# Kernel optimization log

Hardware: AMD Instinct MI355X
Metric: run time of the kernel (lower is better)

## Reference

```python
import jax, jax.numpy as jnp
import numpy as np

DIM = 1024
HEADS = 16


def setup_inputs() -> dict:
    key = jax.random.key(0)
    ks = jax.random.split(key, 9)
    B, N, C = 2, 2048, DIM
    hd = C // HEADS
    s = 1.0 / np.sqrt(C)
    x = jax.random.normal(ks[0], (B, N, C), dtype=jnp.float32)
    wq = jax.random.normal(ks[1], (C, C), dtype=jnp.float32) * s
    wk = jax.random.normal(ks[2], (C, C), dtype=jnp.float32) * s
    wv = jax.random.normal(ks[3], (C, C), dtype=jnp.float32) * s
    wp = jax.random.normal(ks[4], (C, C), dtype=jnp.float32) * s
    bp = jnp.zeros((C,), dtype=jnp.float32)
    # rotary table: angles theta_j = 10000^{-2j/hd}, positions 0..N-1
    inv_freq = 1.0 / (10000.0 ** (jnp.arange(0, hd, 2, dtype=jnp.float32) / hd))
    ang = jnp.arange(N, dtype=jnp.float32)[:, None] * inv_freq[None, :]  # (N, hd//2)
    cos = jnp.cos(ang)
    sin = jnp.sin(ang)
    return {"x": x, "wq": wq, "wk": wk, "wv": wv, "wp": wp, "bp": bp,
            "cos": cos, "sin": sin, "num_heads": HEADS}


def _apply_rotary(t, cos, sin):
    # t: (B, N, H, D); cos/sin: (N, D//2) -> broadcast (1, N, 1, D//2)
    B, N, H, D = t.shape
    tr = t.reshape(B, N, H, D // 2, 2)
    t1, t2 = tr[..., 0], tr[..., 1]
    c = cos[None, :, None, :]
    s = sin[None, :, None, :]
    o1 = t1 * c - t2 * s
    o2 = t1 * s + t2 * c
    return jnp.stack([o1, o2], axis=-1).reshape(B, N, H, D)


def reference(x, wq, wk, wv, wp, bp, cos, sin, num_heads):
    B, N, C = x.shape
    H = num_heads
    D = C // H
    q = (x @ wq.T).reshape(B, N, H, D)
    k = (x @ wk.T).reshape(B, N, H, D)
    v = (x @ wv.T).reshape(B, N, H, D)
    q = _apply_rotary(q, cos, sin)
    k = _apply_rotary(k, cos, sin)
    scale = 1.0 / jnp.sqrt(jnp.asarray(D, dtype=x.dtype))
    # scores: (B, H, N, N)
    scores = jnp.einsum('bnhd,bmhd->bhnm', q, k) * scale
    attn = jax.nn.softmax(scores, axis=-1)
    out = jnp.einsum('bhnm,bmhd->bnhd', attn, v).reshape(B, N, C)
    return out @ wp.T + bp
```

## Files before the change

### kernel.cpp

```cpp
#include <hip/hip_runtime.h>
#include <hip/hip_bf16.h>
#include <stdint.h>

#define DEVI __device__ __forceinline__

using bf16 = __hip_bfloat16;
typedef __bf16 bf16x8 __attribute__((ext_vector_type(8)));
typedef float f32x4 __attribute__((ext_vector_type(4)));
typedef float f32x16 __attribute__((ext_vector_type(16)));
typedef int i32x2 __attribute__((ext_vector_type(2)));

static constexpr int Bb = 2, Nn = 2048, Cc = 1024, Hh = 16, Dd = 64;
static constexpr float CSC = 0.125f * 1.44269504088896340736f;

DEVI bf16 f2bf(float x) { __bf16 h = (__bf16)x; return *(bf16*)&h; }
DEVI float fexp2(float x) { return __builtin_amdgcn_exp2f(x); }

DEVI bf16x8 cvt8(f32x4 a, f32x4 b) {
  bf16x8 r;
  r[0] = (__bf16)a[0]; r[1] = (__bf16)a[1]; r[2] = (__bf16)a[2]; r[3] = (__bf16)a[3];
  r[4] = (__bf16)b[0]; r[5] = (__bf16)b[1]; r[6] = (__bf16)b[2]; r[7] = (__bf16)b[3];
  return r;
}

DEVI uint32_t pk2(float a, float b) {
  __bf16 x = (__bf16)a, y = (__bf16)b;
  uint16_t ux = *(uint16_t*)&x, uy = *(uint16_t*)&y;
  return (uint32_t)ux | ((uint32_t)uy << 16);
}

DEVI bf16x8 mk8(uint32_t a, uint32_t b, uint32_t c, uint32_t d) {
  union { uint32_t u[4]; bf16x8 v; } x;
  x.u[0] = a; x.u[1] = b; x.u[2] = c; x.u[3] = d;
  return x.v;
}

DEVI void gld_lds16(const bf16* g, bf16* l) {
  __builtin_amdgcn_global_load_lds(
      (__attribute__((address_space(1))) void*)(g),
      (__attribute__((address_space(3))) void*)(l),
      16, 0, 0);
}

__global__ __launch_bounds__(256) void k_cvt(const float* __restrict__ x,
                                             const float* __restrict__ wq,
                                             const float* __restrict__ wk,
                                             const float* __restrict__ wv,
                                             const float* __restrict__ wp,
                                             bf16* xb, bf16* wqb, bf16* wkb,
                                             bf16* wvb, bf16* wpb) {
  int bid = blockIdx.x;
  const float* src; bf16* dst; size_t off;
  if (bid < 2048) {
    src = x; dst = xb; off = (size_t)bid * 2048;
  } else {
    int s = (bid - 2048) >> 9, r = (bid - 2048) & 511;
    off = (size_t)r * 2048;
    src = s == 0 ? wq : s == 1 ? wk : s == 2 ? wv : wp;
    dst = s == 0 ? wqb : s == 1 ? wkb : s == 2 ? wvb : wpb;
  }
  size_t i = off + (size_t)threadIdx.x * 8;
  f32x4 a = *(const f32x4*)(src + i);
  f32x4 b = *(const f32x4*)(src + i + 4);
  *(bf16x8*)(dst + i) = cvt8(a, b);
}

template <int MFC, class Epi>
DEVI void gemm_lds_body(const bf16* __restrict__ A, const bf16* __restrict__ Bw,
                        int K, int m0, int n0, bf16* lA, bf16* lB, Epi epi) {
  constexpr int BM = MFC * 32;
  constexpr int PA = BM / 64;
  const int t = threadIdx.x;
  const int lane = t & 63, wave = t >> 6;
  const int wr = wave >> 1, wc = wave & 1;

  f32x4 acc[MFC][4] = {};

  for (int k0 = 0; k0 < K; k0 += 32) {
    __syncthreads();
#pragma unroll
    for (int p = 0; p < PA; ++p) {
      int c = p * 256 + t;
      int row = c >> 2, col = (c & 3) * 8;
      gld_lds16(A + (size_t)(m0 + row) * K + k0 + col,
                lA + (size_t)(p * 256 + wave * 64) * 8);
    }
#pragma unroll
    for (int p = 0; p < 2; ++p) {
      int c = p * 256 + t;
      int row = c >> 2, col = (c & 3) * 8;
      gld_lds16(Bw + (size_t)(n0 + row) * K + k0 + col,
                lB + (size_t)(p * 256 + wave * 64) * 8);
    }
    __syncthreads();

    bf16x8 aF[MFC];
#pragma unroll
    for (int mf = 0; mf < MFC; ++mf)
      aF[mf] = *(const bf16x8*)(lA + (wr * (BM / 2) + mf * 16 + (lane & 15)) * 32 + (lane >> 4) * 8);
#pragma unroll
    for (int nf = 0; nf < 4; ++nf) {
      bf16x8 bF = *(const bf16x8*)(lB + (wc * 64 + nf * 16 + (lane & 15)) * 32 + (lane >> 4) * 8);
#pragma unroll
      for (int mf = 0; mf < MFC; ++mf)
        acc[mf][nf] = __builtin_amdgcn_mfma_f32_16x16x32_bf16(aF[mf], bF, acc[mf][nf], 0, 0, 0);
    }
  }

#pragma unroll
  for (int mf = 0; mf < MFC; ++mf)
#pragma unroll
    for (int nf = 0; nf < 4; ++nf)
#pragma unroll
      for (int r = 0; r < 4; ++r) {
        int gm = m0 + wr * (BM / 2) + mf * 16 + (lane >> 4) * 4 + r;
        int gn = n0 + wc * 64 + nf * 16 + (lane & 15);
        epi(gm, gn, acc[mf][nf][r]);
      }
}

struct EpiRope {
  bf16* dst; const float* cosw; const float* sinw; float scale;
  DEVI void operator()(int gm, int gn, float v) const {
    int b = gm >> 11, n = gm & 2047;
    int h = gn >> 6, d = gn & 63;
    int i = d >> 1;
    float c = cosw[n * 32 + i], s = sinw[n * 32 + i];
    float p = __shfl_xor(v, 1);
    float o = (d & 1) ? (p * s + v * c) : (v * c - p * s);
    dst[((size_t)(b * Hh + h) * Nn + n) * 64 + d] = f2bf(o * scale);
  }
};

struct EpiVt {
  bf16* dst;
  DEVI void operator()(int gm, int gn, float v) const {
    int h = gm >> 6, d = gm & 63;
    int b = gn >> 11, n = gn & 2047;
    dst[((size_t)(b * Hh + h) * 64 + d) * Nn + n] = f2bf(v);
  }
};

struct EpiProj {
  float* dst; const float* bias;
  DEVI void operator()(int gm, int gn, float v) const {
    dst[(size_t)gm * Cc + gn] = v + bias[gn];
  }
};

__global__ __launch_bounds__(256) void k_qkv(const bf16* __restrict__ xb,
                                             const bf16* __restrict__ wqb,
                                             const bf16* __restrict__ wkb,
                                             const bf16* __restrict__ wvb,
                                             bf16* q_ws, bf16* k_ws, bf16* vt_ws,
                                             const float* __restrict__ cw,
                                             const float* __restrict__ sw) {
  __shared__ __align__(16) bf16 smem[256 * 32];
  bf16* lA = smem;
  bf16* lB = smem + 128 * 32;
  int bid = blockIdx.x;
  if (bid < 512) {
    int sub = bid & 255;
    int c = sub & 7, rest = sub >> 3;
    int m0 = (c + 8 * (rest & 3)) * 128;
    int n0 = (rest >> 2) * 128;
    bool isq = bid < 256;
    gemm_lds_body<4>(xb, isq ? wqb : wkb, Cc, m0, n0, lA, lB,
                     EpiRope{isq ? q_ws : k_ws, cw, sw, isq ? CSC : 1.0f});
  } else {
    int sub = bid - 512;
    int c = sub & 7, rest = sub >> 3;
    int n0 = (c + 8 * (rest & 3)) * 128;
    int m0 = (rest >> 2) * 128;
    gemm_lds_body<4>(wvb, xb, Cc, m0, n0, lA, lB, EpiVt{vt_ws});
  }
}

__global__ __launch_bounds__(256) void k_proj(const bf16* __restrict__ A,
                                              const bf16* __restrict__ W,
                                              float* dst, const float* __restrict__ bias) {
  __shared__ __align__(16) bf16 smem[192 * 32];
  gemm_lds_body<2>(A, W, Cc, blockIdx.x * 64, blockIdx.y * 128,
                   smem, smem + 64 * 32, EpiProj{dst, bias});
}

__global__ __launch_bounds__(512) void k_flash(const bf16* __restrict__ q_ws,
                                               const bf16* __restrict__ k_ws,
                                               const bf16* __restrict__ vt_ws,
                                               bf16* __restrict__ attn_o) {
  __shared__ __align__(16) bf16 lK[2][64 * 64];
  __shared__ __align__(16) bf16 lV[2][64 * 64];

  const int t = threadIdx.x, lane = t & 63, wave = t >> 6;
  const int l31 = lane & 31, hi = lane >> 5;
  const int bid = blockIdx.x;
  const int slot = bid >> 3;
  const int bh = (bid & 7) * 4 + (slot >> 3);
  const int q0w = (slot & 7) * 256 + wave * 32;
  const bf16* qg = q_ws + (size_t)bh * Nn * 64;
  const bf16* kg = k_ws + (size_t)bh * Nn * 64;
  const bf16* vg = vt_ws + (size_t)bh * 64 * Nn;

  bf16x8 qF[4];
#pragma unroll
  for (int kd = 0; kd < 4; ++kd)
    qF[kd] = *(const bf16x8*)(qg + (size_t)(q0w + l31) * 64 + kd * 16 + hi * 8);

  f32x16 accO[2] = {};
  float Ls4[4] = {};

  auto stage_tile = [&](int kt, int buf) {
    int row = t >> 3, cis = (t & 7) ^ (row & 7);
    gld_lds16(kg + (size_t)(kt * 64 + row) * 64 + cis * 8,
              lK[buf] + (size_t)(wave * 64) * 8);
    gld_lds16(vg + (size_t)row * Nn + kt * 64 + cis * 8,
              lV[buf] + (size_t)(wave * 64) * 8);
  };

  stage_tile(0, 0);
  __syncthreads();

  constexpr int NT = Nn / 64;
  for (int kt = 0; kt < NT; ++kt) {
    const int cur = kt & 1;
    if (kt + 1 < NT) stage_tile(kt + 1, cur ^ 1);

#pragma unroll
    for (int kb = 0; kb < 2; ++kb) {
      f32x16 accT = {};
      __builtin_amdgcn_s_setprio(1);
#pragma unroll
      for (int kd = 0; kd < 4; ++kd) {
        int row = kb * 32 + l31;
        bf16x8 kF = *(const bf16x8*)(lK[cur] +
            ((row * 64 + kd * 16 + hi * 8) ^ ((row & 7) << 3)));
        accT = __builtin_amdgcn_mfma_f32_32x32x16_bf16(kF, qF[kd], accT, 0, 0, 0);
      }
      __builtin_amdgcn_s_setprio(0);

      float p[16];
#pragma unroll
      for (int r = 0; r < 16; ++r) { p[r] = fexp2(accT[r]); Ls4[r & 3] += p[r]; }

      uint32_t c01 = pk2(p[0], p[1]),  c23 = pk2(p[2], p[3]);
      uint32_t c89 = pk2(p[4], p[5]),  cab = pk2(p[6], p[7]);
      uint32_t d01 = pk2(p[8], p[9]),  d23 = pk2(p[10], p[11]);
      uint32_t d89 = pk2(p[12], p[13]), dab = pk2(p[14], p[15]);
      i32x2 s0a = __builtin_amdgcn_permlane32_swap((int)c01, (int)c89, false, false);
      i32x2 s0b = __builtin_amdgcn_permlane32_swap((int)c23, (int)cab, false, false);
      i32x2 s1a = __builtin_amdgcn_permlane32_swap((int)d01, (int)d89, false, false);
      i32x2 s1b = __builtin_amdgcn_permlane32_swap((int)d23, (int)dab, false, false);
      bf16x8 paF[2] = { mk8(s0a[0], s0b[0], s0a[1], s0b[1]),
                        mk8(s1a[0], s1b[0], s1a[1], s1b[1]) };

      __builtin_amdgcn_s_setprio(1);
#pragma unroll
      for (int d0 = 0; d0 < 2; ++d0)
#pragma unroll
        for (int s = 0; s < 2; ++s) {
          int vrow = d0 * 32 + l31;
          bf16x8 vF = *(const bf16x8*)(lV[cur] +
              ((vrow * 64 + kb * 32 + s * 16 + hi * 8) ^ ((vrow & 7) << 3)));
          accO[d0] = __builtin_amdgcn_mfma_f32_32x32x16_bf16(paF[s], vF, accO[d0], 0, 0, 0);
        }
      __builtin_amdgcn_s_setprio(0);
    }

    __syncthreads();
  }

  float L = (Ls4[0] + Ls4[1]) + (Ls4[2] + Ls4[3]);
  L += __shfl_xor(L, 32);

  const int b = bh >> 4, h = bh & 15;
#pragma unroll
  for (int r = 0; r < 16; ++r) {
    int ql = (r & 3) + 8 * (r >> 2) + 4 * hi;
    float inv = 1.0f / __shfl(L, ql);
    int qrow = q0w + ql;
#pragma unroll
    for (int d0 = 0; d0 < 2; ++d0) {
      int d = d0 * 32 + l31;
      attn_o[((size_t)(b * Nn + qrow)) * Cc + h * 64 + d] = f2bf(accO[d0][r] * inv);
    }
  }
}

extern "C" void kernel_launch(void* const* d_in, const int* in_sizes, int n_in,
                              void* d_out, int out_size, void* d_ws, size_t ws_size,
                              hipStream_t stream) {
  (void)in_sizes; (void)n_in; (void)out_size; (void)ws_size;
  const float* x  = (const float*)d_in[0];
  const float* wq = (const float*)d_in[1];
  const float* wk = (const float*)d_in[2];
  const float* wv = (const float*)d_in[3];
  const float* wp = (const float*)d_in[4];
  const float* bp = (const float*)d_in[5];
  const float* cw = (const float*)d_in[6];
  const float* sw = (const float*)d_in[7];
  float* out = (float*)d_out;

  const size_t M1 = 1u << 20;
  bf16* x_bf  = (bf16*)d_ws;
  bf16* wq_bf = x_bf + 4 * M1;
  bf16* wk_bf = wq_bf + M1;
  bf16* wv_bf = wk_bf + M1;
  bf16* wp_bf = wv_bf + M1;
  bf16* q_ws  = wp_bf + M1;
  bf16* k_ws  = q_ws + 4 * M1;
  bf16* vt_ws = k_ws + 4 * M1;
  bf16* ao_ws = x_bf;

  k_cvt  <<<dim3(4096),    dim3(256), 0, stream>>>(x, wq, wk, wv, wp,
                                                   x_bf, wq_bf, wk_bf, wv_bf, wp_bf);
  k_qkv  <<<dim3(768),     dim3(256), 0, stream>>>(x_bf, wq_bf, wk_bf, wv_bf,
                                                   q_ws, k_ws, vt_ws, cw, sw);
  k_flash<<<dim3(256),     dim3(512), 0, stream>>>(q_ws, k_ws, vt_ws, ao_ws);
  k_proj <<<dim3(64, 8),   dim3(256), 0, stream>>>(ao_ws, wp_bf, out, bp);
}
```

Before: 122.9 us.

## Fuse x fp32-to-bf16 conversion into QKV GEMM and enlarge flash K/V tiles

The separate conversion pass over the activation x is dropped. The QKV GEMM now reads fp32 x directly, converts it to bf16 in registers and prefetches the next k-slice into registers before storing it to LDS. The flash-attention kernel also doubles its K/V tile from 64 to 128 keys per stage, which halves the number of barrier and stage iterations at the cost of twice the LDS use. The trade-offs are that x is re-read in fp32 by many GEMM blocks, doubling that read traffic, and that the higher LDS footprint may reduce occupancy.

Measured after the change: 121.6 us. No clear change (-1.0%).

```diff
diff --git a/kernel.cpp b/kernel.cpp
--- a/kernel.cpp
+++ b/kernel.cpp
@@ -42,57 +42,96 @@
       16, 0, 0);
 }
 
-__global__ __launch_bounds__(256) void k_cvt(const float* __restrict__ x,
-                                             const float* __restrict__ wq,
+__global__ __launch_bounds__(256) void k_cvt(const float* __restrict__ wq,
                                              const float* __restrict__ wk,
                                              const float* __restrict__ wv,
                                              const float* __restrict__ wp,
-                                             bf16* xb, bf16* wqb, bf16* wkb,
+                                             bf16* wqb, bf16* wkb,
                                              bf16* wvb, bf16* wpb) {
   int bid = blockIdx.x;
-  const float* src; bf16* dst; size_t off;
-  if (bid < 2048) {
-    src = x; dst = xb; off = (size_t)bid * 2048;
-  } else {
-    int s = (bid - 2048) >> 9, r = (bid - 2048) & 511;
-    off = (size_t)r * 2048;
-    src = s == 0 ? wq : s == 1 ? wk : s == 2 ? wv : wp;
-    dst = s == 0 ? wqb : s == 1 ? wkb : s == 2 ? wvb : wpb;
-  }
+  int s = bid >> 9, r = bid & 511;
+  size_t off = (size_t)r * 2048;
+  const float* src = s == 0 ? wq : s == 1 ? wk : s == 2 ? wv : wp;
+  bf16* dst = s == 0 ? wqb : s == 1 ? wkb : s == 2 ? wvb : wpb;
   size_t i = off + (size_t)threadIdx.x * 8;
   f32x4 a = *(const f32x4*)(src + i);
   f32x4 b = *(const f32x4*)(src + i + 4);
   *(bf16x8*)(dst + i) = cvt8(a, b);
 }
 
-template <int MFC, class Epi>
-DEVI void gemm_lds_body(const bf16* __restrict__ A, const bf16* __restrict__ Bw,
-                        int K, int m0, int n0, bf16* lA, bf16* lB, Epi epi) {
+template <int MFC, bool AF32, bool BF32, class Epi>
+DEVI void gemm_body2(const void* Ap, const void* Bp, int K, int m0, int n0,
+                     bf16* lA, bf16* lB, Epi epi) {
   constexpr int BM = MFC * 32;
   constexpr int PA = BM / 64;
   const int t = threadIdx.x;
   const int lane = t & 63, wave = t >> 6;
   const int wr = wave >> 1, wc = wave & 1;
 
-  f32x4 acc[MFC][4] = {};
-
-  for (int k0 = 0; k0 < K; k0 += 32) {
-    __syncthreads();
+  bf16x8 ra[PA], rb[2];
+  auto loadA = [&](int k0) {
 #pragma unroll
     for (int p = 0; p < PA; ++p) {
       int c = p * 256 + t;
       int row = c >> 2, col = (c & 3) * 8;
-      gld_lds16(A + (size_t)(m0 + row) * K + k0 + col,
-                lA + (size_t)(p * 256 + wave * 64) * 8);
-    }
+      const float* pa = (const float*)Ap + (size_t)(m0 + row) * K + k0 + col;
+      ra[p] = cvt8(*(const f32x4*)pa, *(const f32x4*)(pa + 4));
+    }
+  };
+  auto loadB = [&](int k0) {
 #pragma unroll
     for (int p = 0; p < 2; ++p) {
       int c = p * 256 + t;
       int row = c >> 2, col = (c & 3) * 8;
-      gld_lds16(Bw + (size_t)(n0 + row) * K + k0 + col,
-                lB + (size_t)(p * 256 + wave * 64) * 8);
-    }
+      const float* pb = (const float*)Bp + (size_t)(n0 + row) * K + k0 + col;
+      rb[p] = cvt8(*(const f32x4*)pb, *(const f32x4*)(pb + 4));
+    }
+  };
+
+  f32x4 acc[MFC][4] = {};
+  if constexpr (AF32) loadA(0);
+  if constexpr (BF32) loadB(0);
+
+  const int NS = K / 32;
+  for (int s = 0; s < NS; ++s) {
+    const int k0 = s * 32;
     __syncthreads();
+    if constexpr (AF32) {
+#pragma unroll
+      for (int p = 0; p < PA; ++p) {
+        int c = p * 256 + t;
+        *(bf16x8*)(lA + (c >> 2) * 32 + (c & 3) * 8) = ra[p];
+      }
+    } else {
+#pragma unroll
+      for (int p = 0; p < PA; ++p) {
+        int c = p * 256 + t;
+        int row = c >> 2, col = (c & 3) * 8;
+        gld_lds16((const bf16*)Ap + (size_t)(m0 + row) * K + k0 + col,
+                  lA + (size_t)(p * 256 + wave * 64) * 8);
+      }
+    }
+    if constexpr (BF32) {
+#pragma unroll
+      for (int p = 0; p < 2; ++p) {
+        int c = p * 256 + t;
+        *(bf16x8*)(lB + (c >> 2) * 32 + (c & 3) * 8) = rb[p];
+      }
+    } else {
+#pragma unroll
+      for (int p = 0; p < 2; ++p) {
+        int c = p * 256 + t;
+        int row = c >> 2, col = (c & 3) * 8;
+        gld_lds16((const bf16*)Bp + (size_t)(n0 + row) * K + k0 + col,
+                  lB + (size_t)(p * 256 + wave * 64) * 8);
+      }
+    }
+    __syncthreads();
+
+    if (s + 1 < NS) {
+      if constexpr (AF32) loadA(k0 + 32);
+      if constexpr (BF32) loadB(k0 + 32);
+    }
 
     bf16x8 aF[MFC];
 #pragma unroll
@@ -148,7 +187,7 @@
   }
 };
 
-__global__ __launch_bounds__(256) void k_qkv(const bf16* __restrict__ xb,
+__global__ __launch_bounds__(256) void k_qkv(const float* __restrict__ x,
                                              const bf16* __restrict__ wqb,
                                              const bf16* __restrict__ wkb,
                                              const bf16* __restrict__ wvb,
@@ -165,14 +204,14 @@
     int m0 = (c + 8 * (rest & 3)) * 128;
     int n0 = (rest >> 2) * 128;
     bool isq = bid < 256;
-    gemm_lds_body<4>(xb, isq ? wqb : wkb, Cc, m0, n0, lA, lB,
-                     EpiRope{isq ? q_ws : k_ws, cw, sw, isq ? CSC : 1.0f});
+    gemm_body2<4, true, false>(x, isq ? wqb : wkb, Cc, m0, n0, lA, lB,
+                               EpiRope{isq ? q_ws : k_ws, cw, sw, isq ? CSC : 1.0f});
   } else {
     int sub = bid - 512;
     int c = sub & 7, rest = sub >> 3;
     int n0 = (c + 8 * (rest & 3)) * 128;
     int m0 = (rest >> 2) * 128;
-    gemm_lds_body<4>(wvb, xb, Cc, m0, n0, lA, lB, EpiVt{vt_ws});
+    gemm_body2<4, false, true>(wvb, x, Cc, m0, n0, lA, lB, EpiVt{vt_ws});
   }
 }
 
@@ -180,16 +219,16 @@
                                               const bf16* __restrict__ W,
                                               float* dst, const float* __restrict__ bias) {
   __shared__ __align__(16) bf16 smem[192 * 32];
-  gemm_lds_body<2>(A, W, Cc, blockIdx.x * 64, blockIdx.y * 128,
-                   smem, smem + 64 * 32, EpiProj{dst, bias});
+  gemm_body2<2, false, false>(A, W, Cc, blockIdx.x * 64, blockIdx.y * 128,
+                              smem, smem + 64 * 32, EpiProj{dst, bias});
 }
 
 __global__ __launch_bounds__(512) void k_flash(const bf16* __restrict__ q_ws,
                                                const bf16* __restrict__ k_ws,
                                                const bf16* __restrict__ vt_ws,
                                                bf16* __restrict__ attn_o) {
-  __shared__ __align__(16) bf16 lK[2][64 * 64];
-  __shared__ __align__(16) bf16 lV[2][64 * 64];
+  __shared__ __align__(16) bf16 lK[2][128 * 64];
+  __shared__ __align__(16) bf16 lV[2][64 * 128];
 
   const int t = threadIdx.x, lane = t & 63, wave = t >> 6;
   const int l31 = lane & 31, hi = lane >> 5;
@@ -210,30 +249,35 @@
   float Ls4[4] = {};
 
   auto stage_tile = [&](int kt, int buf) {
-    int row = t >> 3, cis = (t & 7) ^ (row & 7);
-    gld_lds16(kg + (size_t)(kt * 64 + row) * 64 + cis * 8,
-              lK[buf] + (size_t)(wave * 64) * 8);
-    gld_lds16(vg + (size_t)row * Nn + kt * 64 + cis * 8,
-              lV[buf] + (size_t)(wave * 64) * 8);
+#pragma unroll
+    for (int p = 0; p < 2; ++p) {
+      int c = p * 512 + t;
+      int krow = c >> 3, kch = (c & 7) ^ (krow & 7);
+      gld_lds16(kg + (size_t)(kt * 128 + krow) * 64 + kch * 8,
+                lK[buf] + (size_t)(p * 512 + wave * 64) * 8);
+      int vrow = c >> 4, vch = (c & 15) ^ (vrow & 7);
+      gld_lds16(vg + (size_t)vrow * Nn + kt * 128 + vch * 8,
+                lV[buf] + (size_t)(p * 512 + wave * 64) * 8);
+    }
   };
 
   stage_tile(0, 0);
   __syncthreads();
 
-  constexpr int NT = Nn / 64;
+  constexpr int NT = Nn / 128;
   for (int kt = 0; kt < NT; ++kt) {
     const int cur = kt & 1;
     if (kt + 1 < NT) stage_tile(kt + 1, cur ^ 1);
 
 #pragma unroll
-    for (int kb = 0; kb < 2; ++kb) {
+    for (int kb = 0; kb < 4; ++kb) {
       f32x16 accT = {};
       __builtin_amdgcn_s_setprio(1);
 #pragma unroll
       for (int kd = 0; kd < 4; ++kd) {
         int row = kb * 32 + l31;
-        bf16x8 kF = *(const bf16x8*)(lK[cur] +
-            ((row * 64 + kd * 16 + hi * 8) ^ ((row & 7) << 3)));
+        int ch = (kd * 2 + hi) ^ (row & 7);
+        bf16x8 kF = *(const bf16x8*)(lK[cur] + row * 64 + ch * 8);
         accT = __builtin_amdgcn_mfma_f32_32x32x16_bf16(kF, qF[kd], accT, 0, 0, 0);
       }
       __builtin_amdgcn_s_setprio(0);
@@ -259,8 +303,8 @@
 #pragma unroll
         for (int s = 0; s < 2; ++s) {
           int vrow = d0 * 32 + l31;
-          bf16x8 vF = *(const bf16x8*)(lV[cur] +
-              ((vrow * 64 + kb * 32 + s * 16 + hi * 8) ^ ((vrow & 7) << 3)));
+          int ch = (kb * 4 + s * 2 + hi) ^ (vrow & 7);
+          bf16x8 vF = *(const bf16x8*)(lV[cur] + vrow * 128 + ch * 8);
           accO[d0] = __builtin_amdgcn_mfma_f32_32x32x16_bf16(paF[s], vF, accO[d0], 0, 0, 0);
         }
       __builtin_amdgcn_s_setprio(0);
@@ -301,19 +345,18 @@
   float* out = (float*)d_out;
 
   const size_t M1 = 1u << 20;
-  bf16* x_bf  = (bf16*)d_ws;
-  bf16* wq_bf = x_bf + 4 * M1;
+  bf16* ao_ws = (bf16*)d_ws;
+  bf16* wq_bf = ao_ws + 4 * M1;
   bf16* wk_bf = wq_bf + M1;
   bf16* wv_bf = wk_bf + M1;
   bf16* wp_bf = wv_bf + M1;
   bf16* q_ws  = wp_bf + M1;
   bf16* k_ws  = q_ws + 4 * M1;
   bf16* vt_ws = k_ws + 4 * M1;
-  bf16* ao_ws = x_bf;
-
-  k_cvt  <<<dim3(4096),    dim3(256), 0, stream>>>(x, wq, wk, wv, wp,
-                                                   x_bf, wq_bf, wk_bf, wv_bf, wp_bf);
-  k_qkv  <<<dim3(768),     dim3(256), 0, stream>>>(x_bf, wq_bf, wk_bf, wv_bf,
+
+  k_cvt  <<<dim3(2048),    dim3(256), 0, stream>>>(wq, wk, wv, wp,
+                                                   wq_bf, wk_bf, wv_bf, wp_bf);
+  k_qkv  <<<dim3(768),     dim3(256), 0, stream>>>(x, wq_bf, wk_bf, wv_bf,
                                                    q_ws, k_ws, vt_ws, cw, sw);
   k_flash<<<dim3(256),     dim3(512), 0, stream>>>(q_ws, k_ws, vt_ws, ao_ws);
   k_proj <<<dim3(64, 8),   dim3(256), 0, stream>>>(ao_ws, wp_bf, out, bp);
```
